# Performance work log

Measured on AMD Instinct MI355X. Metric: run time of the kernel, lower is better.

Reference implementation:

```python
import jax, jax.numpy as jnp
import numpy as np

B, C_IN, T = 16, 1, 10240
C = 256                # conv_dim_out == config.model.conv_channels
KERNEL, STRIDE, PAD = 10, 5, 0
K_STEPS = 12           # config.model.predict_steps
NEG = 10               # config.train.neg_samples
EPS = 1e-5
L_OUT = (T + 2 * PAD - KERNEL) // STRIDE + 1   # 2047


def setup_inputs() -> dict:
    key = jax.random.key(0)
    ks = jax.random.split(key, 5)
    return {
        "x": jax.random.normal(ks[0], (B, C_IN, T), jnp.float32),
        "conv_w": jax.random.normal(ks[1], (C, C_IN, KERNEL), jnp.float32) * 0.1,
        "conv_b": jnp.zeros((C,), jnp.float32),
        "bn_gamma": jnp.ones((C,), jnp.float32),
        "bn_beta": jnp.zeros((C,), jnp.float32),
        "tr_w": jax.random.normal(ks[2], (K_STEPS, C, C), jnp.float32) / np.sqrt(C).astype(np.float32),
        "tr_b": jnp.zeros((K_STEPS, C), jnp.float32),
        "perm": jax.random.permutation(ks[3], L_OUT),  # randperm over the time axis
    }


def reference(x, conv_w, conv_b, bn_gamma, bn_beta, tr_w, tr_b, perm):
    # ---- encoder: Conv1d -> ReLU -> BatchNorm1d (training-mode batch stats) ----
    h = jax.lax.conv_general_dilated(
        x, conv_w, window_strides=(STRIDE,), padding=[(PAD, PAD)],
        dimension_numbers=("NCH", "OIH", "NCH"))
    h = jax.nn.relu(h + conv_b[None, :, None])            # (B, C, L)
    mu = h.mean(axis=(0, 2), keepdims=True)
    var = h.var(axis=(0, 2), keepdims=True)               # biased, as torch BN
    h = (h - mu) * jax.lax.rsqrt(var + EPS)
    h = h * bn_gamma[None, :, None] + bn_beta[None, :, None]
    z = h.transpose(0, 2, 1)                              # (B, L, C)

    # ---- negatives: batch-roll by 1, random permutation of the time axis; detached ----
    z_negative = jax.lax.stop_gradient(jnp.roll(z, 1, axis=0)[:, perm, :])

    L = z.shape[1]
    # z_neg_full[b, i] == roll(z_neg, i, axis=0)[b] == z_neg[(b - i) % B]
    roll_idx = (jnp.arange(B)[:, None] - jnp.arange(NEG)[None, :]) % B  # (B, NEG)

    losses = []
    for k in range(1, K_STEPS + 1):
        l_len = L - k
        z_pos = z[:, k:, :]                               # (B, l, C)
        z_neg = z_negative[:, k:, :]                      # (B, l, C)
        z_neg_full = z_neg[roll_idx]                      # (B, NEG, l, C)
        W, bb = tr_w[k - 1], tr_b[k - 1]
        est_pos = (z_pos @ W + bb)[:, None]               # (B, 1, l, C)
        est_neg = z_neg_full @ W + bb                     # (B, NEG, l, C)
        estimated = jnp.concatenate([est_pos, est_neg], axis=1)        # (B, S, l, C)
        z_full = jnp.concatenate([z_pos[:, None], z_neg_full], axis=1)  # (B, S, l, C)
        f = jnp.einsum("bslc,bslc->bsl", estimated, z_full)
        # faithful to torch: flatten (b, s, l) row-major then view as (b*l, S)
        f_k = f.reshape(B * l_len, NEG + 1)
        logp = jax.nn.log_softmax(f_k, axis=1)
        losses.append(-logp.sum() / ((l_len - k) * B))

    # torch forward returns z.permute(0, 2, 1); losses returned too for baseline use
    return z.transpose(0, 2, 1), jnp.stack(losses)
```

## Files before the change

### kernel.cpp

```cpp
#include <hip/hip_runtime.h>
#include <hip/hip_bf16.h>
#include <math.h>

constexpr int B_ = 16;
constexpr int T_ = 10240;
constexpr int C_ = 256;
constexpr int KW = 10;
constexpr int L_ = 2047;
constexpr int N_ = B_ * L_;
constexpr int KSTEPS = 12;
constexpr float EPS_ = 1e-5f;
constexpr int ZSTR = 264;
constexpr int QSTR = 32768;

typedef short bf16x8 __attribute__((ext_vector_type(8)));
typedef float f32x4  __attribute__((ext_vector_type(4)));

__global__ __launch_bounds__(256) void conv_stats_kernel(
    const float* __restrict__ x, const float* __restrict__ cw,
    const float* __restrict__ cb, float* __restrict__ ssum, float* __restrict__ ssq)
{
    const int b  = blockIdx.y;
    const int l0 = blockIdx.x * 128;
    const int cnt = min(128, L_ - l0);
    const int c = threadIdx.x;
    __shared__ float xs[128 * 5 + 8];
    const float* xb = x + (size_t)b * T_;
    for (int i = threadIdx.x; i < cnt * 5 + 5; i += 256) xs[i] = xb[l0 * 5 + i];
    float w[KW];
#pragma unroll
    for (int j = 0; j < KW; ++j) w[j] = cw[c * KW + j];
    const float bias = cb[c];
    __syncthreads();
    float s = 0.f, s2 = 0.f;
    for (int dl = 0; dl < cnt; ++dl) {
        float v = bias;
#pragma unroll
        for (int j = 0; j < KW; ++j) v = fmaf(xs[dl * 5 + j], w[j], v);
        v = fmaxf(v, 0.f);
        s += v;
        s2 = fmaf(v, v, s2);
    }
    atomicAdd(&ssum[c], s);
    atomicAdd(&ssq[c], s2);
}

__global__ void bn_finalize_kernel(const float* __restrict__ ssum, const float* __restrict__ ssq,
                                   const float* __restrict__ gamma, const float* __restrict__ beta,
                                   float* __restrict__ scale, float* __restrict__ shift)
{
    int c = threadIdx.x;
    const float inv_n = 1.0f / (float)N_;
    float mu  = ssum[c] * inv_n;
    float var = ssq[c] * inv_n - mu * mu;
    float sc  = gamma[c] * rsqrtf(var + EPS_);
    scale[c] = sc;
    shift[c] = beta[c] - mu * sc;
}

__global__ __launch_bounds__(256) void conv_norm_kernel(
    const float* __restrict__ x, const float* __restrict__ cw, const float* __restrict__ cb,
    const float* __restrict__ scale, const float* __restrict__ shift,
    __hip_bfloat16* __restrict__ Zb, float* __restrict__ out0)
{
    const int b  = blockIdx.y;
    const int l0 = blockIdx.x * 64;
    const int cnt = min(64, L_ - l0);
    const int c = threadIdx.x;
    __shared__ float xs[64 * 5 + 16];
    __shared__ float zt[64][261];
    const float* xb = x + (size_t)b * T_;
    for (int i = threadIdx.x; i < cnt * 5 + 5; i += 256) xs[i] = xb[l0 * 5 + i];
    float w[KW];
#pragma unroll
    for (int j = 0; j < KW; ++j) w[j] = cw[c * KW + j];
    const float bias = cb[c];
    const float sc = scale[c], sh = shift[c];
    __syncthreads();
    for (int dl = 0; dl < cnt; ++dl) {
        float v = bias;
#pragma unroll
        for (int j = 0; j < KW; ++j) v = fmaf(xs[dl * 5 + j], w[j], v);
        v = fmaxf(v, 0.f);
        float z = fmaf(v, sc, sh);
        int l = l0 + dl;
        Zb[((size_t)(b * L_ + l)) * C_ + c] = __float2bfloat16(z);
        zt[dl][c] = z;
    }
    __syncthreads();
    const int l4  = threadIdx.x & 15;
    const int crb = threadIdx.x >> 4;
#pragma unroll
    for (int seg = 0; seg < 4; ++seg) {
        int ll = seg * 16 + l4;
        bool valid = ll < cnt;
#pragma unroll
        for (int i = 0; i < 16; ++i) {
            int cr = crb + 16 * i;
            if (valid)
                out0[((size_t)(b * C_ + cr)) * L_ + l0 + ll] = zt[ll][cr];
        }
    }
}

__global__ __launch_bounds__(256) void wt_kernel(const float* __restrict__ tw,
                                                 __hip_bfloat16* __restrict__ Wt)
{
    const int k  = blockIdx.z;
    const int c0 = blockIdx.x * 64, j0 = blockIdx.y * 64;
    __shared__ float tile[64][65];
    for (int i = threadIdx.x; i < 64 * 64; i += 256) {
        int c = i >> 6, j = i & 63;
        tile[c][j] = tw[((size_t)k * C_ + (c0 + c)) * C_ + j0 + j];
    }
    __syncthreads();
    for (int i = threadIdx.x; i < 64 * 64; i += 256) {
        int j = i >> 6, c = i & 63;
        Wt[((size_t)k * C_ + (j0 + j)) * C_ + c0 + c] = __float2bfloat16(tile[c][j]);
    }
}

__global__ __launch_bounds__(256, 2) void qmfma_kernel(
    const __hip_bfloat16* __restrict__ Zb, const __hip_bfloat16* __restrict__ Wt,
    const float* __restrict__ tb, float* __restrict__ qt)
{
    const int k   = blockIdx.y;
    const int grp = blockIdx.x;
    const __hip_bfloat16* __restrict__ Wk = Wt + (size_t)k * C_ * C_;

    __shared__ __hip_bfloat16 zs[2][32 * ZSTR];
    __shared__ float qacc[4][256];

    const int tid  = threadIdx.x;
    const int lane = tid & 63, wave = tid >> 6;
    const int n16  = lane & 15, quad = lane >> 4;

    bf16x8 wfrag[4][8];
    {
        const __hip_bfloat16* wb = Wk + ((size_t)(64 * wave + n16)) * C_ + quad * 8;
#pragma unroll
        for (int ct = 0; ct < 4; ++ct)
#pragma unroll
            for (int it = 0; it < 8; ++it)
                wfrag[ct][it] = *(const bf16x8*)(wb + ct * 16 * C_ + it * 32);
    }
    float4 bias4[4];
#pragma unroll
    for (int ct = 0; ct < 4; ++ct)
        bias4[ct] = *(const float4*)(tb + k * C_ + 64 * wave + ct * 16 + quad * 4);

    const int row0 = grp * 8 * 32;
    float4 greg[4];

#pragma unroll
    for (int i = 0; i < 4; ++i) {
        int chunk = tid + i * 256;
        int r = chunk >> 5, c16 = chunk & 31;
        int rg = row0 + r; if (rg > N_ - 1) rg = N_ - 1;
        greg[i] = *(const float4*)(Zb + (size_t)rg * C_ + c16 * 8);
    }
#pragma unroll
    for (int i = 0; i < 4; ++i) {
        int chunk = tid + i * 256;
        int r = chunk >> 5, c16 = chunk & 31;
        *(float4*)((__hip_bfloat16*)zs[0] + r * ZSTR + c16 * 8) = greg[i];
    }
    __syncthreads();

    for (int t = 0; t < 8; ++t) {
        const int p = t & 1;

        if (t < 7) {
            int r0 = row0 + (t + 1) * 32;
#pragma unroll
            for (int i = 0; i < 4; ++i) {
                int chunk = tid + i * 256;
                int r = chunk >> 5, c16 = chunk & 31;
                int rg = r0 + r; if (rg > N_ - 1) rg = N_ - 1;
                greg[i] = *(const float4*)(Zb + (size_t)rg * C_ + c16 * 8);
            }
        }

        f32x4 acc[2][4];
#pragma unroll
        for (int rt = 0; rt < 2; ++rt)
#pragma unroll
            for (int ct = 0; ct < 4; ++ct) acc[rt][ct] = f32x4{0.f, 0.f, 0.f, 0.f};

        const __hip_bfloat16* zb0 = (const __hip_bfloat16*)zs[p] + n16 * ZSTR + quad * 8;
#pragma unroll
        for (int it = 0; it < 8; ++it) {
            bf16x8 zf0 = *(const bf16x8*)(zb0 + it * 32);
            bf16x8 zf1 = *(const bf16x8*)(zb0 + 16 * ZSTR + it * 32);
#pragma unroll
            for (int ct = 0; ct < 4; ++ct) {
                acc[0][ct] = __builtin_amdgcn_mfma_f32_16x16x32_bf16(
                    wfrag[ct][it], zf0, acc[0][ct], 0, 0, 0);
                acc[1][ct] = __builtin_amdgcn_mfma_f32_16x16x32_bf16(
                    wfrag[ct][it], zf1, acc[1][ct], 0, 0, 0);
            }
        }

#pragma unroll
        for (int rt = 0; rt < 2; ++rt) {
            float s = 0.f;
#pragma unroll
            for (int ct = 0; ct < 4; ++ct) {
                const __hip_bfloat16* zp = (const __hip_bfloat16*)zs[p]
                    + (rt * 16 + n16) * ZSTR + 64 * wave + ct * 16 + quad * 4;
                uint2 zz = *(const uint2*)zp;
                float z0 = __uint_as_float(zz.x << 16);
                float z1 = __uint_as_float(zz.x & 0xffff0000u);
                float z2 = __uint_as_float(zz.y << 16);
                float z3 = __uint_as_float(zz.y & 0xffff0000u);
                s = fmaf(acc[rt][ct][0] + bias4[ct].x, z0, s);
                s = fmaf(acc[rt][ct][1] + bias4[ct].y, z1, s);
                s = fmaf(acc[rt][ct][2] + bias4[ct].z, z2, s);
                s = fmaf(acc[rt][ct][3] + bias4[ct].w, z3, s);
            }
            s += __shfl_xor(s, 16);
            s += __shfl_xor(s, 32);
            if (lane < 16) qacc[wave][t * 32 + rt * 16 + n16] = s;
        }

        if (t < 7) {
#pragma unroll
            for (int i = 0; i < 4; ++i) {
                int chunk = tid + i * 256;
                int r = chunk >> 5, c16 = chunk & 31;
                *(float4*)((__hip_bfloat16*)zs[1 - p] + r * ZSTR + c16 * 8) = greg[i];
            }
        }
        __syncthreads();
    }

    {
        int r  = tid;
        int rg = row0 + r;
        if (rg < N_) {
            float qv = qacc[0][r] + qacc[1][r] + qacc[2][r] + qacc[3][r];
            int b = rg / L_;
            int l = rg - b * L_;
            qt[(size_t)k * QSTR + (l << 4) + b] = qv;
        }
    }
}

__global__ __launch_bounds__(256) void loss_kernel(
    const float* __restrict__ qt, const int* __restrict__ perm, float* __restrict__ lacc)
{
    const int k = blockIdx.y + 1;
    const float* qk = qt + (size_t)(k - 1) * QSTR;
    const int nval = B_ * (L_ - k);
    const int idx = blockIdx.x * 256 + threadIdx.x;

    float contrib = 0.f;
    if (idx < nval) {
        int b = idx & 15;
        int l = k + (idx >> 4);
        float f0 = qk[(l << 4) | b];
        int pl = perm[l];
        const float* qn = qk + ((size_t)pl << 4);
        float f[10];
#pragma unroll
        for (int n = 0; n < 10; ++n) f[n] = qn[(b + 15 - n) & 15];
        float m = f0;
#pragma unroll
        for (int i = 0; i < 10; ++i) m = fmaxf(m, f[i]);
        float se = expf(f0 - m), fs = f0;
#pragma unroll
        for (int i = 0; i < 10; ++i) { se += expf(f[i] - m); fs += f[i]; }
        contrib = 11.f * (m + logf(se)) - fs;
    }

    __shared__ float red[4];
#pragma unroll
    for (int off = 32; off > 0; off >>= 1) contrib += __shfl_down(contrib, off);
    const int lane = threadIdx.x & 63;
    const int wave = threadIdx.x >> 6;
    if (lane == 0) red[wave] = contrib;
    __syncthreads();
    if (threadIdx.x == 0) atomicAdd(&lacc[k - 1], red[0] + red[1] + red[2] + red[3]);
}

__global__ void finalize_loss_kernel(const float* __restrict__ lacc, float* __restrict__ out1)
{
    int k = threadIdx.x;
    if (k < KSTEPS) {
        float div = (float)((L_ - 2 * (k + 1)) * B_);
        out1[k] = lacc[k] / div;
    }
}

extern "C" void kernel_launch(void* const* d_in, const int* in_sizes, int n_in,
                              void* d_out, int out_size, void* d_ws, size_t ws_size,
                              hipStream_t stream)
{
    const float* x     = (const float*)d_in[0];
    const float* cw    = (const float*)d_in[1];
    const float* cb    = (const float*)d_in[2];
    const float* gamma = (const float*)d_in[3];
    const float* beta  = (const float*)d_in[4];
    const float* tw    = (const float*)d_in[5];
    const float* tb    = (const float*)d_in[6];
    const int*   perm  = (const int*)d_in[7];

    float* out0 = (float*)d_out;
    float* out1 = out0 + (size_t)B_ * C_ * L_;

    char* ws = (char*)d_ws;
    __hip_bfloat16* Zb = (__hip_bfloat16*)ws;   ws += (size_t)N_ * C_ * 2;
    __hip_bfloat16* Wt = (__hip_bfloat16*)ws;   ws += (size_t)KSTEPS * C_ * C_ * 2;
    float* qt    = (float*)ws;                  ws += (size_t)KSTEPS * QSTR * 4;
    float* ssum  = (float*)ws;                  ws += C_ * 4;
    float* ssq   = (float*)ws;                  ws += C_ * 4;
    float* lacc  = (float*)ws;                  ws += 64 * 4;
    float* scale = (float*)ws;                  ws += C_ * 4;
    float* shift = (float*)ws;                  ws += C_ * 4;

    hipMemsetAsync(ssum, 0, (C_ + C_ + 64) * sizeof(float), stream);

    dim3 gstat(16, 16);
    conv_stats_kernel<<<gstat, 256, 0, stream>>>(x, cw, cb, ssum, ssq);
    bn_finalize_kernel<<<1, 256, 0, stream>>>(ssum, ssq, gamma, beta, scale, shift);

    dim3 gcv(32, 16);
    conv_norm_kernel<<<gcv, 256, 0, stream>>>(x, cw, cb, scale, shift, Zb, out0);

    dim3 gwt(4, 4, KSTEPS);
    wt_kernel<<<gwt, 256, 0, stream>>>(tw, Wt);

    dim3 gq(128, KSTEPS);
    qmfma_kernel<<<gq, 256, 0, stream>>>(Zb, Wt, tb, qt);

    dim3 gl(128, KSTEPS);
    loss_kernel<<<gl, 256, 0, stream>>>(qt, perm, lacc);
    finalize_loss_kernel<<<1, 64, 0, stream>>>(lacc, out1);
}
```

Measured before the change: 204.1 us.

## Fuse weight transpose into stats kernel, swizzle LDS, shrink conv_norm tiles

Merges the conv statistics kernel and the weight-transpose kernel into one launch, using block-index ranges to dispatch. The conv_norm kernel now uses 32-row tiles and doubles its grid, which gives more blocks and less shared memory per block. The transposed output write is reorganised so each thread writes 32 channels for one time index. In the MFMA kernel, the padded LDS row stride is replaced by an XOR swizzle on 16-byte chunks to avoid bank conflicts while cutting LDS size. This saves one launch and some LDS, at the cost of more index arithmetic.

```diff
diff --git a/kernel.cpp b/kernel.cpp
--- a/kernel.cpp
+++ b/kernel.cpp
@@ -10,39 +10,57 @@
 constexpr int N_ = B_ * L_;
 constexpr int KSTEPS = 12;
 constexpr float EPS_ = 1e-5f;
-constexpr int ZSTR = 264;
 constexpr int QSTR = 32768;
 
 typedef short bf16x8 __attribute__((ext_vector_type(8)));
 typedef float f32x4  __attribute__((ext_vector_type(4)));
 
-__global__ __launch_bounds__(256) void conv_stats_kernel(
-    const float* __restrict__ x, const float* __restrict__ cw,
-    const float* __restrict__ cb, float* __restrict__ ssum, float* __restrict__ ssq)
-{
-    const int b  = blockIdx.y;
-    const int l0 = blockIdx.x * 128;
-    const int cnt = min(128, L_ - l0);
-    const int c = threadIdx.x;
-    __shared__ float xs[128 * 5 + 8];
-    const float* xb = x + (size_t)b * T_;
-    for (int i = threadIdx.x; i < cnt * 5 + 5; i += 256) xs[i] = xb[l0 * 5 + i];
-    float w[KW];
-#pragma unroll
-    for (int j = 0; j < KW; ++j) w[j] = cw[c * KW + j];
-    const float bias = cb[c];
-    __syncthreads();
-    float s = 0.f, s2 = 0.f;
-    for (int dl = 0; dl < cnt; ++dl) {
-        float v = bias;
-#pragma unroll
-        for (int j = 0; j < KW; ++j) v = fmaf(xs[dl * 5 + j], w[j], v);
-        v = fmaxf(v, 0.f);
-        s += v;
-        s2 = fmaf(v, v, s2);
-    }
-    atomicAdd(&ssum[c], s);
-    atomicAdd(&ssq[c], s2);
+__global__ __launch_bounds__(256) void stats_wt_kernel(
+    const float* __restrict__ x, const float* __restrict__ cw, const float* __restrict__ cb,
+    float* __restrict__ ssum, float* __restrict__ ssq,
+    const float* __restrict__ tw, __hip_bfloat16* __restrict__ Wt)
+{
+    __shared__ float smem[64 * 65];
+    const int bid = blockIdx.x;
+    if (bid < 256) {
+        const int b  = bid & 15;
+        const int l0 = (bid >> 4) * 128;
+        const int cnt = min(128, L_ - l0);
+        const int c = threadIdx.x;
+        float* xs = smem;
+        const float* xb = x + (size_t)b * T_;
+        for (int i = threadIdx.x; i < cnt * 5 + 5; i += 256) xs[i] = xb[l0 * 5 + i];
+        float w[KW];
+#pragma unroll
+        for (int j = 0; j < KW; ++j) w[j] = cw[c * KW + j];
+        const float bias = cb[c];
+        __syncthreads();
+        float s = 0.f, s2 = 0.f;
+        for (int dl = 0; dl < cnt; ++dl) {
+            float v = bias;
+#pragma unroll
+            for (int j = 0; j < KW; ++j) v = fmaf(xs[dl * 5 + j], w[j], v);
+            v = fmaxf(v, 0.f);
+            s += v;
+            s2 = fmaf(v, v, s2);
+        }
+        atomicAdd(&ssum[c], s);
+        atomicAdd(&ssq[c], s2);
+    } else {
+        const int idx = bid - 256;
+        const int k  = idx >> 4;
+        const int c0 = ((idx & 15) >> 2) * 64, j0 = (idx & 3) * 64;
+        float (*tile)[65] = (float(*)[65])smem;
+        for (int i = threadIdx.x; i < 64 * 64; i += 256) {
+            int c = i >> 6, j = i & 63;
+            tile[c][j] = tw[((size_t)k * C_ + (c0 + c)) * C_ + j0 + j];
+        }
+        __syncthreads();
+        for (int i = threadIdx.x; i < 64 * 64; i += 256) {
+            int j = i >> 6, c = i & 63;
+            Wt[((size_t)k * C_ + (j0 + j)) * C_ + c0 + c] = __float2bfloat16(tile[c][j]);
+        }
+    }
 }
 
 __global__ void bn_finalize_kernel(const float* __restrict__ ssum, const float* __restrict__ ssq,
@@ -64,11 +82,11 @@
     __hip_bfloat16* __restrict__ Zb, float* __restrict__ out0)
 {
     const int b  = blockIdx.y;
-    const int l0 = blockIdx.x * 64;
-    const int cnt = min(64, L_ - l0);
+    const int l0 = blockIdx.x * 32;
+    const int cnt = min(32, L_ - l0);
     const int c = threadIdx.x;
-    __shared__ float xs[64 * 5 + 16];
-    __shared__ float zt[64][261];
+    __shared__ float xs[32 * 5 + 8];
+    __shared__ float zt[32][257];
     const float* xb = x + (size_t)b * T_;
     for (int i = threadIdx.x; i < cnt * 5 + 5; i += 256) xs[i] = xb[l0 * 5 + i];
     float w[KW];
@@ -83,40 +101,18 @@
         for (int j = 0; j < KW; ++j) v = fmaf(xs[dl * 5 + j], w[j], v);
         v = fmaxf(v, 0.f);
         float z = fmaf(v, sc, sh);
-        int l = l0 + dl;
-        Zb[((size_t)(b * L_ + l)) * C_ + c] = __float2bfloat16(z);
+        Zb[((size_t)(b * L_ + l0 + dl)) * C_ + c] = __float2bfloat16(z);
         zt[dl][c] = z;
     }
     __syncthreads();
-    const int l4  = threadIdx.x & 15;
-    const int crb = threadIdx.x >> 4;
-#pragma unroll
-    for (int seg = 0; seg < 4; ++seg) {
-        int ll = seg * 16 + l4;
-        bool valid = ll < cnt;
-#pragma unroll
-        for (int i = 0; i < 16; ++i) {
-            int cr = crb + 16 * i;
-            if (valid)
-                out0[((size_t)(b * C_ + cr)) * L_ + l0 + ll] = zt[ll][cr];
-        }
-    }
-}
-
-__global__ __launch_bounds__(256) void wt_kernel(const float* __restrict__ tw,
-                                                 __hip_bfloat16* __restrict__ Wt)
-{
-    const int k  = blockIdx.z;
-    const int c0 = blockIdx.x * 64, j0 = blockIdx.y * 64;
-    __shared__ float tile[64][65];
-    for (int i = threadIdx.x; i < 64 * 64; i += 256) {
-        int c = i >> 6, j = i & 63;
-        tile[c][j] = tw[((size_t)k * C_ + (c0 + c)) * C_ + j0 + j];
-    }
-    __syncthreads();
-    for (int i = threadIdx.x; i < 64 * 64; i += 256) {
-        int j = i >> 6, c = i & 63;
-        Wt[((size_t)k * C_ + (j0 + j)) * C_ + c0 + c] = __float2bfloat16(tile[c][j]);
+    const int lq  = threadIdx.x & 31;
+    const int cr0 = threadIdx.x >> 5;
+    if (lq < cnt) {
+#pragma unroll
+        for (int i = 0; i < 32; ++i) {
+            int cr = cr0 * 32 + i;
+            out0[((size_t)(b * C_ + cr)) * L_ + l0 + lq] = zt[lq][cr];
+        }
     }
 }
 
@@ -128,12 +124,13 @@
     const int grp = blockIdx.x;
     const __hip_bfloat16* __restrict__ Wk = Wt + (size_t)k * C_ * C_;
 
-    __shared__ __hip_bfloat16 zs[2][32 * ZSTR];
+    __shared__ __hip_bfloat16 zs[2][32 * 256];
     __shared__ float qacc[4][256];
 
     const int tid  = threadIdx.x;
     const int lane = tid & 63, wave = tid >> 6;
     const int n16  = lane & 15, quad = lane >> 4;
+    const int sw   = n16 & 7;
 
     bf16x8 wfrag[4][8];
     {
@@ -155,15 +152,15 @@
 #pragma unroll
     for (int i = 0; i < 4; ++i) {
         int chunk = tid + i * 256;
-        int r = chunk >> 5, c16 = chunk & 31;
+        int r = chunk >> 5;
         int rg = row0 + r; if (rg > N_ - 1) rg = N_ - 1;
-        greg[i] = *(const float4*)(Zb + (size_t)rg * C_ + c16 * 8);
+        greg[i] = *(const float4*)(Zb + (size_t)rg * C_ + (chunk & 31) * 8);
     }
 #pragma unroll
     for (int i = 0; i < 4; ++i) {
         int chunk = tid + i * 256;
-        int r = chunk >> 5, c16 = chunk & 31;
-        *(float4*)((__hip_bfloat16*)zs[0] + r * ZSTR + c16 * 8) = greg[i];
+        int r = chunk >> 5, j = chunk & 31;
+        *(float4*)((__hip_bfloat16*)zs[0] + r * 256 + (j ^ (r & 7)) * 8) = greg[i];
     }
     __syncthreads();
 
@@ -175,9 +172,9 @@
 #pragma unroll
             for (int i = 0; i < 4; ++i) {
                 int chunk = tid + i * 256;
-                int r = chunk >> 5, c16 = chunk & 31;
+                int r = chunk >> 5;
                 int rg = r0 + r; if (rg > N_ - 1) rg = N_ - 1;
-                greg[i] = *(const float4*)(Zb + (size_t)rg * C_ + c16 * 8);
+                greg[i] = *(const float4*)(Zb + (size_t)rg * C_ + (chunk & 31) * 8);
             }
         }
 
@@ -187,11 +184,12 @@
 #pragma unroll
             for (int ct = 0; ct < 4; ++ct) acc[rt][ct] = f32x4{0.f, 0.f, 0.f, 0.f};
 
-        const __hip_bfloat16* zb0 = (const __hip_bfloat16*)zs[p] + n16 * ZSTR + quad * 8;
+        const __hip_bfloat16* zsp = (const __hip_bfloat16*)zs[p];
 #pragma unroll
         for (int it = 0; it < 8; ++it) {
-            bf16x8 zf0 = *(const bf16x8*)(zb0 + it * 32);
-            bf16x8 zf1 = *(const bf16x8*)(zb0 + 16 * ZSTR + it * 32);
+            const int js = (it * 4 + quad) ^ sw;
+            bf16x8 zf0 = *(const bf16x8*)(zsp + n16 * 256 + js * 8);
+            bf16x8 zf1 = *(const bf16x8*)(zsp + (n16 + 16) * 256 + js * 8);
 #pragma unroll
             for (int ct = 0; ct < 4; ++ct) {
                 acc[0][ct] = __builtin_amdgcn_mfma_f32_16x16x32_bf16(
@@ -203,11 +201,12 @@
 
 #pragma unroll
         for (int rt = 0; rt < 2; ++rt) {
+            const int row = rt * 16 + n16;
             float s = 0.f;
 #pragma unroll
             for (int ct = 0; ct < 4; ++ct) {
-                const __hip_bfloat16* zp = (const __hip_bfloat16*)zs[p]
-                    + (rt * 16 + n16) * ZSTR + 64 * wave + ct * 16 + quad * 4;
+                const int j  = 8 * wave + 2 * ct + (quad >> 1);
+                const char* zp = (const char*)zsp + row * 512 + ((j ^ sw) << 4) + (quad & 1) * 8;
                 uint2 zz = *(const uint2*)zp;
                 float z0 = __uint_as_float(zz.x << 16);
                 float z1 = __uint_as_float(zz.x & 0xffff0000u);
@@ -220,15 +219,15 @@
             }
             s += __shfl_xor(s, 16);
             s += __shfl_xor(s, 32);
-            if (lane < 16) qacc[wave][t * 32 + rt * 16 + n16] = s;
+            if (lane < 16) qacc[wave][t * 32 + row] = s;
         }
 
         if (t < 7) {
 #pragma unroll
             for (int i = 0; i < 4; ++i) {
                 int chunk = tid + i * 256;
-                int r = chunk >> 5, c16 = chunk & 31;
-                *(float4*)((__hip_bfloat16*)zs[1 - p] + r * ZSTR + c16 * 8) = greg[i];
+                int r = chunk >> 5, j = chunk & 31;
+                *(float4*)((__hip_bfloat16*)zs[1 - p] + r * 256 + (j ^ (r & 7)) * 8) = greg[i];
             }
         }
         __syncthreads();
@@ -320,15 +319,11 @@
 
     hipMemsetAsync(ssum, 0, (C_ + C_ + 64) * sizeof(float), stream);
 
-    dim3 gstat(16, 16);
-    conv_stats_kernel<<<gstat, 256, 0, stream>>>(x, cw, cb, ssum, ssq);
+    stats_wt_kernel<<<448, 256, 0, stream>>>(x, cw, cb, ssum, ssq, tw, Wt);
     bn_finalize_kernel<<<1, 256, 0, stream>>>(ssum, ssq, gamma, beta, scale, shift);
 
-    dim3 gcv(32, 16);
+    dim3 gcv(64, 16);
     conv_norm_kernel<<<gcv, 256, 0, stream>>>(x, cw, cb, scale, shift, Zb, out0);
-
-    dim3 gwt(4, 4, KSTEPS);
-    wt_kernel<<<gwt, 256, 0, stream>>>(tw, Wt);
 
     dim3 gq(128, KSTEPS);
     qmfma_kernel<<<gq, 256, 0, stream>>>(Zb, Wt, tb, qt);
```

Result: faster. 191.9 us (-6.0%).
